# Performance work log

Measured on AMD Instinct MI355X. Metric: run time of the kernel, lower is better.

## Reference

```python
import jax, jax.numpy as jnp
import numpy as np

D_MODEL = 1024
N_HEADS = 16
HEAD_DIM = D_MODEL // N_HEADS


def setup_inputs() -> dict:
    key = jax.random.key(0)
    ks = jax.random.split(key, 5)
    x = jax.random.normal(ks[0], (2, 2048, D_MODEL), dtype=jnp.float32)
    s = 1.0 / np.sqrt(D_MODEL)
    W_qkv = jax.random.normal(ks[1], (D_MODEL, 3 * D_MODEL), dtype=jnp.float32) * s
    b_qkv = jnp.zeros((3 * D_MODEL,), dtype=jnp.float32)
    W_proj = jax.random.normal(ks[2], (D_MODEL, D_MODEL), dtype=jnp.float32) * s
    b_proj = jnp.zeros((D_MODEL,), dtype=jnp.float32)
    return {"x": x, "W_qkv": W_qkv, "b_qkv": b_qkv, "W_proj": W_proj, "b_proj": b_proj}


def reference(x, W_qkv, b_qkv, W_proj, b_proj):
    b, t, c = x.shape
    qkv = x @ W_qkv + b_qkv  # [b,t,3c]
    q, k, v = jnp.split(qkv, 3, axis=-1)
    # [b, h, t, d]
    q = q.reshape(b, t, N_HEADS, HEAD_DIM).transpose(0, 2, 1, 3)
    k = k.reshape(b, t, N_HEADS, HEAD_DIM).transpose(0, 2, 1, 3)
    v = v.reshape(b, t, N_HEADS, HEAD_DIM).transpose(0, 2, 1, 3)
    att = jnp.einsum('bhqd,bhkd->bhqk', q, k) / np.sqrt(HEAD_DIM)
    causal = jnp.tril(jnp.ones((t, t), dtype=bool))  # [t,t]
    att = jnp.where(causal[None, None], att, -jnp.inf)
    att = jax.nn.softmax(att, axis=-1)
    out = jnp.einsum('bhqk,bhkd->bhqd', att, v)  # [b,h,t,d]
    out = out.transpose(0, 2, 1, 3).reshape(b, t, c)
    return out @ W_proj + b_proj
```

## Files before the change

kernel.cpp:

```cpp
#include <hip/hip_runtime.h>
#include <hip/hip_bf16.h>

#define NB 2
#define NH 16
#define HD 64
#define DM 1024
#define TT 2048

typedef __attribute__((ext_vector_type(4))) float f32x4;
typedef __attribute__((ext_vector_type(8))) short bf16x8;

__device__ __forceinline__ unsigned short f2bf(float f) {
  union { float f; unsigned int i; } x; x.f = f;
  unsigned int r = x.i + 0x7fffu + ((x.i >> 16) & 1u);
  return (unsigned short)(r >> 16);
}

__device__ __forceinline__ unsigned int cvtpk(float lo, float hi) {
  unsigned int r;
  asm("v_cvt_pk_bf16_f32 %0, %1, %2" : "=v"(r) : "v"(lo), "v"(hi));
  return r;
}

__device__ __forceinline__ void async16(unsigned short* lds_base, const unsigned short* g) {
  __builtin_amdgcn_global_load_lds(
      (const __attribute__((address_space(1))) void*)g,
      (__attribute__((address_space(3))) void*)lds_base, 16, 0, 0);
}

__global__ __launch_bounds__(256)
void prep_kernel(const float* __restrict__ x, unsigned short* __restrict__ xbf,
                 const float* __restrict__ Wqkv, unsigned short* __restrict__ WqkvT,
                 const float* __restrict__ Wproj, unsigned short* __restrict__ WprojT)
{
  __shared__ unsigned short T[64][72];
  const int bid = blockIdx.x;
  const int t = threadIdx.x;

  if (bid < 2048) {
    const int i = bid * 256 + t;
    const f32x4 a = *(const f32x4*)(x + (size_t)i * 8);
    const f32x4 b = *(const f32x4*)(x + (size_t)i * 8 + 4);
    uint4 o;
    o.x = f2bf(a.x) | ((unsigned)f2bf(a.y) << 16);
    o.y = f2bf(a.z) | ((unsigned)f2bf(a.w) << 16);
    o.z = f2bf(b.x) | ((unsigned)f2bf(b.y) << 16);
    o.w = f2bf(b.z) | ((unsigned)f2bf(b.w) << 16);
    *(uint4*)(xbf + (size_t)i * 8) = o;
    return;
  }

  const float* W;
  unsigned short* WT;
  int n0, k0, N;
  if (bid < 2048 + 768) {
    const int li = bid - 2048;
    W = Wqkv; WT = WqkvT; N = 3 * DM;
    n0 = (li % 48) * 64; k0 = (li / 48) * 64;
  } else {
    const int li = bid - 2816;
    W = Wproj; WT = WprojT; N = DM;
    n0 = (li % 16) * 64; k0 = (li / 16) * 64;
  }
  const int r = t >> 2;
  const int c = (t & 3) * 16;
  const float* src = W + (size_t)(k0 + r) * N + n0 + c;
  #pragma unroll
  for (int s = 0; s < 4; ++s) {
    const f32x4 v = *(const f32x4*)(src + s * 4);
    T[c + s*4 + 0][r] = f2bf(v.x);
    T[c + s*4 + 1][r] = f2bf(v.y);
    T[c + s*4 + 2][r] = f2bf(v.z);
    T[c + s*4 + 3][r] = f2bf(v.w);
  }
  __syncthreads();
  unsigned short* dst = WT + (size_t)(n0 + r) * DM + k0 + c;
  *(uint4*)(dst)     = *(const uint4*)(&T[r][c]);
  *(uint4*)(dst + 8) = *(const uint4*)(&T[r][c + 8]);
}

template<int MODE>
__global__ __launch_bounds__(256)
void gemm_bf16(const unsigned short* __restrict__ A, const unsigned short* __restrict__ BT,
               const float* __restrict__ bias, void* __restrict__ Cout,
               int M, int N, int K)
{
  __shared__ unsigned short As[128 * 32];
  __shared__ unsigned short Bs[128 * 32];
  const int tid = threadIdx.x;
  const int lane = tid & 63;
  const int w = tid >> 6;
  const int wr = w >> 1, wc = w & 1;
  const int l15 = lane & 15, g = lane >> 4;

  const int gx = gridDim.x;
  const int li = blockIdx.y * gx + blockIdx.x;
  const int chunk = (gx * gridDim.y) >> 3;
  const int tile = (li & 7) * chunk + (li >> 3);
  const int m0 = (tile / gx) * 128;
  const int n0 = (tile % gx) * 128;

  f32x4 acc[4][4] = {};

  const int ar0 = tid >> 2,          as0 = (tid & 3) * 8;
  const int ar1 = (256 + tid) >> 2;
  const unsigned short* A0 = A + (size_t)(m0 + ar0) * K + as0;
  const unsigned short* A1 = A + (size_t)(m0 + ar1) * K + as0;
  const unsigned short* B0 = BT + (size_t)(n0 + ar0) * K + as0;
  const unsigned short* B1 = BT + (size_t)(n0 + ar1) * K + as0;
  unsigned short* AsW0 = &As[(0 * 256 + w * 64) * 8];
  unsigned short* AsW1 = &As[(1 * 256 + w * 64) * 8];
  unsigned short* BsW0 = &Bs[(0 * 256 + w * 64) * 8];
  unsigned short* BsW1 = &Bs[(1 * 256 + w * 64) * 8];

  for (int k0 = 0; k0 < K; k0 += 32) {
    async16(AsW0, A0 + k0);
    async16(AsW1, A1 + k0);
    async16(BsW0, B0 + k0);
    async16(BsW1, B1 + k0);
    __syncthreads();

    bf16x8 af[4], bfv[4];
    #pragma unroll
    for (int i = 0; i < 4; ++i)
      af[i] = *(const bf16x8*)(&As[(wr * 64 + i * 16 + l15) * 32 + g * 8]);
    #pragma unroll
    for (int j = 0; j < 4; ++j)
      bfv[j] = *(const bf16x8*)(&Bs[(wc * 64 + j * 16 + l15) * 32 + g * 8]);
    #pragma unroll
    for (int i = 0; i < 4; ++i)
      #pragma unroll
      for (int j = 0; j < 4; ++j)
        acc[i][j] = __builtin_amdgcn_mfma_f32_16x16x32_bf16(af[i], bfv[j], acc[i][j], 0, 0, 0);
    __syncthreads();
  }

  #pragma unroll
  for (int i = 0; i < 4; ++i) {
    #pragma unroll
    for (int j = 0; j < 4; ++j) {
      #pragma unroll
      for (int e = 0; e < 4; ++e) {
        const int row = m0 + wr * 64 + i * 16 + g * 4 + e;
        const int col = n0 + wc * 64 + j * 16 + l15;
        float val = acc[i][j][e] + bias[col];
        if (MODE == 0) {
          const int which = col >> 10;
          if (which == 0) val *= 0.125f;
          const int rem = col & 1023;
          const int hh = rem >> 6, dd = rem & 63;
          const int bb = row >> 11, tt = row & 2047;
          ((unsigned short*)Cout)[((((size_t)which * NB + bb) * NH + hh) * TT + tt) * HD + dd] = f2bf(val);
        } else {
          ((float*)Cout)[(size_t)row * N + col] = val;
        }
      }
    }
  }
}

__global__ __launch_bounds__(512)
void attn_kernel(const unsigned short* __restrict__ qkv, unsigned short* __restrict__ attn_out)
{
  __shared__ unsigned short Ksm[64 * 72];
  __shared__ unsigned short VTsm[64 * 70];
  __shared__ unsigned short Psm[8][32 * 72];

  const int tid = threadIdx.x;
  const int lane = tid & 63;
  const int wv = tid >> 6;
  const int l15 = lane & 15;
  const int g = lane >> 4;

  const int li = blockIdx.x;
  const int xcd = li & 7;
  const int j = li >> 3;
  const int bh = ((j >> 3) << 3) | xcd;
  const int ip = j & 7;

  const int qlo0 = ip * 128;
  const int qhi0 = (15 - ip) * 128;

  const size_t base = (size_t)bh * TT * HD;
  const unsigned short* Qg = qkv + base;
  const unsigned short* Kg = qkv + (size_t)NB * NH * TT * HD + base;
  const unsigned short* Vg = qkv + (size_t)2 * NB * NH * TT * HD + base;

  const int qw_lo = qlo0 + wv * 16;
  const int qw_hi = qhi0 + wv * 16;
  const bf16x8 qlf0 = *(const bf16x8*)(Qg + (size_t)(qw_lo + l15) * HD + g * 8);
  const bf16x8 qlf1 = *(const bf16x8*)(Qg + (size_t)(qw_lo + l15) * HD + 32 + g * 8);
  const bf16x8 qhf0 = *(const bf16x8*)(Qg + (size_t)(qw_hi + l15) * HD + g * 8);
  const bf16x8 qhf1 = *(const bf16x8*)(Qg + (size_t)(qw_hi + l15) * HD + 32 + g * 8);

  f32x4 olo[4] = {}, ohi[4] = {};
  float llo = 0.f, lhi = 0.f;

  const bool kRole = (wv < 4);
  const int krow = (tid & 255) >> 2;
  const int kseg = (tid & 3) * 16;
  const int vt   = tid & 255;
  const int vr0  = (vt >> 4) * 4;
  const int vc0  = (vt & 15) * 4;

  const int nt    = 32 - 2 * ip;
  const int lo_nt = 2 * ip + 2;

  uint4 st0, st1;
  {
    if (kRole) {
      const unsigned short* kp = Kg + (size_t)krow * HD + kseg;
      st0 = *(const uint4*)(kp);
      st1 = *(const uint4*)(kp + 8);
    } else {
      const uint2 a = *(const uint2*)(Vg + (size_t)(vr0 + 0) * HD + vc0);
      const uint2 b = *(const uint2*)(Vg + (size_t)(vr0 + 1) * HD + vc0);
      const uint2 c = *(const uint2*)(Vg + (size_t)(vr0 + 2) * HD + vc0);
      const uint2 d = *(const uint2*)(Vg + (size_t)(vr0 + 3) * HD + vc0);
      st0.x = a.x; st0.y = a.y; st0.z = b.x; st0.w = b.y;
      st1.x = c.x; st1.y = c.y; st1.z = d.x; st1.w = d.y;
    }
  }

  for (int t = 0; t < nt; ++t) {
    const int t0 = t * 64;
    const bool lo_act = (t < lo_nt);
    __syncthreads();
    if (kRole) {
      *(uint4*)(&Ksm[krow * 72 + kseg])     = st0;
      *(uint4*)(&Ksm[krow * 72 + kseg + 8]) = st1;
    } else {
      unsigned short r0[4] = {(unsigned short)(st0.x & 0xffffu), (unsigned short)(st0.x >> 16),
                              (unsigned short)(st0.y & 0xffffu), (unsigned short)(st0.y >> 16)};
      unsigned short r1[4] = {(unsigned short)(st0.z & 0xffffu), (unsigned short)(st0.z >> 16),
                              (unsigned short)(st0.w & 0xffffu), (unsigned short)(st0.w >> 16)};
      unsigned short r2[4] = {(unsigned short)(st1.x & 0xffffu), (unsigned short)(st1.x >> 16),
                              (unsigned short)(st1.y & 0xffffu), (unsigned short)(st1.y >> 16)};
      unsigned short r3[4] = {(unsigned short)(st1.z & 0xffffu), (unsigned short)(st1.z >> 16),
                              (unsigned short)(st1.w & 0xffffu), (unsigned short)(st1.w >> 16)};
      #pragma unroll
      for (int c2 = 0; c2 < 4; ++c2) {
        ushort4 col;
        col.x = r0[c2]; col.y = r1[c2]; col.z = r2[c2]; col.w = r3[c2];
        *(ushort4*)(&VTsm[(vc0 + c2) * 70 + vr0]) = col;
      }
    }
    __syncthreads();

    if (t + 1 < nt) {
      const int t1 = t0 + 64;
      if (kRole) {
        const unsigned short* kp = Kg + (size_t)(t1 + krow) * HD + kseg;
        st0 = *(const uint4*)(kp);
        st1 = *(const uint4*)(kp + 8);
      } else {
        const uint2 a = *(const uint2*)(Vg + (size_t)(t1 + vr0 + 0) * HD + vc0);
        const uint2 b = *(const uint2*)(Vg + (size_t)(t1 + vr0 + 1) * HD + vc0);
        const uint2 c = *(const uint2*)(Vg + (size_t)(t1 + vr0 + 2) * HD + vc0);
        const uint2 d = *(const uint2*)(Vg + (size_t)(t1 + vr0 + 3) * HD + vc0);
        st0.x = a.x; st0.y = a.y; st0.z = b.x; st0.w = b.y;
        st1.x = c.x; st1.y = c.y; st1.z = d.x; st1.w = d.y;
      }
    }

    f32x4 shiT[4] = {}, sloT[4] = {};
    __builtin_amdgcn_s_setprio(1);
    #pragma unroll
    for (int b = 0; b < 4; ++b) {
      const bf16x8 kf0 = *(const bf16x8*)(&Ksm[(b * 16 + l15) * 72 + g * 8]);
      const bf16x8 kf1 = *(const bf16x8*)(&Ksm[(b * 16 + l15) * 72 + 32 + g * 8]);
      shiT[b] = __builtin_amdgcn_mfma_f32_16x16x32_bf16(kf0, qhf0, shiT[b], 0, 0, 0);
      shiT[b] = __builtin_amdgcn_mfma_f32_16x16x32_bf16(kf1, qhf1, shiT[b], 0, 0, 0);
      if (lo_act) {
        sloT[b] = __builtin_amdgcn_mfma_f32_16x16x32_bf16(kf0, qlf0, sloT[b], 0, 0, 0);
        sloT[b] = __builtin_amdgcn_mfma_f32_16x16x32_bf16(kf1, qlf1, sloT[b], 0, 0, 0);
      }
    }
    __builtin_amdgcn_s_setprio(0);

    if (t0 + 63 > qw_hi) {
      #pragma unroll
      for (int b = 0; b < 4; ++b)
        #pragma unroll
        for (int e = 0; e < 4; ++e)
          if (t0 + b * 16 + 4 * g + e > qw_hi + l15) shiT[b][e] = -INFINITY;
    }
    if (lo_act && t0 + 63 > qw_lo) {
      #pragma unroll
      for (int b = 0; b < 4; ++b)
        #pragma unroll
        for (int e = 0; e < 4; ++e)
          if (t0 + b * 16 + 4 * g + e > qw_lo + l15) sloT[b][e] = -INFINITY;
    }

    #pragma unroll
    for (int b = 0; b < 4; ++b) {
      const float p0 = __expf(shiT[b][0]);
      const float p1 = __expf(shiT[b][1]);
      const float p2 = __expf(shiT[b][2]);
      const float p3 = __expf(shiT[b][3]);
      lhi += (p0 + p1) + (p2 + p3);
      uint2 wd; wd.x = cvtpk(p0, p1); wd.y = cvtpk(p2, p3);
      *(uint2*)(&Psm[wv][(16 + l15) * 72 + b * 16 + 4 * g]) = wd;
    }
    if (lo_act) {
      #pragma unroll
      for (int b = 0; b < 4; ++b) {
        const float p0 = __expf(sloT[b][0]);
        const float p1 = __expf(sloT[b][1]);
        const float p2 = __expf(sloT[b][2]);
        const float p3 = __expf(sloT[b][3]);
        llo += (p0 + p1) + (p2 + p3);
        uint2 wd; wd.x = cvtpk(p0, p1); wd.y = cvtpk(p2, p3);
        *(uint2*)(&Psm[wv][l15 * 72 + b * 16 + 4 * g]) = wd;
      }
    }

    __builtin_amdgcn_s_setprio(1);
    #pragma unroll
    for (int c = 0; c < 2; ++c) {
      const bf16x8 pfh = *(const bf16x8*)(&Psm[wv][(16 + l15) * 72 + c * 32 + g * 8]);
      bf16x8 pfl;
      if (lo_act) pfl = *(const bf16x8*)(&Psm[wv][l15 * 72 + c * 32 + g * 8]);
      #pragma unroll
      for (int db = 0; db < 4; ++db) {
        const bf16x8 vf = *(const bf16x8*)(&VTsm[(db * 16 + l15) * 70 + c * 32 + g * 8]);
        ohi[db] = __builtin_amdgcn_mfma_f32_16x16x32_bf16(pfh, vf, ohi[db], 0, 0, 0);
        if (lo_act) olo[db] = __builtin_amdgcn_mfma_f32_16x16x32_bf16(pfl, vf, olo[db], 0, 0, 0);
      }
    }
    __builtin_amdgcn_s_setprio(0);
  }

  lhi += __shfl_xor(lhi, 16, 64);
  lhi += __shfl_xor(lhi, 32, 64);
  llo += __shfl_xor(llo, 16, 64);
  llo += __shfl_xor(llo, 32, 64);

  const int bb = bh >> 4;
  const int hh = bh & 15;
  #pragma unroll
  for (int e = 0; e < 4; ++e) {
    const float invh = 1.f / __shfl(lhi, 4 * g + e, 64);
    const float invl = 1.f / __shfl(llo, 4 * g + e, 64);
    const int qh = qw_hi + 4 * g + e;
    const int ql = qw_lo + 4 * g + e;
    #pragma unroll
    for (int db = 0; db < 4; ++db) {
      attn_out[(size_t)(bb * TT + qh) * DM + hh * HD + db * 16 + l15] = f2bf(ohi[db][e] * invh);
      attn_out[(size_t)(bb * TT + ql) * DM + hh * HD + db * 16 + l15] = f2bf(olo[db][e] * invl);
    }
  }
}

extern "C" void kernel_launch(void* const* d_in, const int* in_sizes, int n_in,
                              void* d_out, int out_size, void* d_ws, size_t ws_size,
                              hipStream_t stream)
{
  const float* x     = (const float*)d_in[0];
  const float* Wqkv  = (const float*)d_in[1];
  const float* bqkv  = (const float*)d_in[2];
  const float* Wproj = (const float*)d_in[3];
  const float* bproj = (const float*)d_in[4];

  const size_t qkv_elems = (size_t)3 * NB * NH * TT * HD;
  unsigned short* qkv_ws  = (unsigned short*)d_ws;
  unsigned short* WqkvT   = qkv_ws + qkv_elems;
  unsigned short* WprojT  = WqkvT + (size_t)3 * DM * DM;
  unsigned short* xbf     = WprojT + (size_t)DM * DM;
  unsigned short* attn_ws = xbf;

  hipLaunchKernelGGL(prep_kernel, dim3(3072, 1, 1), dim3(256), 0, stream,
                     x, xbf, Wqkv, WqkvT, Wproj, WprojT);
  hipLaunchKernelGGL((gemm_bf16<0>), dim3(3 * DM / 128, NB * TT / 128, 1), dim3(256), 0, stream,
                     xbf, WqkvT, bqkv, (void*)qkv_ws, NB * TT, 3 * DM, DM);
  hipLaunchKernelGGL(attn_kernel, dim3(256, 1, 1), dim3(512), 0, stream,
                     qkv_ws, attn_ws);
  hipLaunchKernelGGL((gemm_bf16<1>), dim3(DM / 128, NB * TT / 128, 1), dim3(256), 0, stream,
                     attn_ws, WprojT, bproj, d_out, NB * TT, DM, DM);
}
```

Baseline: 133.9 us.

## Split paired causal query tiles into separate blocks and skip fully masked key tiles

The attention kernel used to give each block a low and a high 128-row query tile so causal work was balanced. Now each block handles one query tile, the grid doubles to 512 blocks, and the heavy tiles are scheduled first. Each wave also skips the QK/PV work for key tiles that lie entirely above its own 16 rows. This adds parallelism and removes masked compute, but the K/V tiles are loaded into LDS twice as often overall, and block costs become uneven.

```diff
diff --git a/kernel.cpp b/kernel.cpp
--- a/kernel.cpp
+++ b/kernel.cpp
@@ -164,7 +164,7 @@
 {
   __shared__ unsigned short Ksm[64 * 72];
   __shared__ unsigned short VTsm[64 * 70];
-  __shared__ unsigned short Psm[8][32 * 72];
+  __shared__ unsigned short Psm[8][16 * 72];
 
   const int tid = threadIdx.x;
   const int lane = tid & 63;
@@ -174,27 +174,25 @@
 
   const int li = blockIdx.x;
   const int xcd = li & 7;
-  const int j = li >> 3;
+  const int r = li >> 3;
+  const int halfid = r >> 5;
+  const int j = r & 31;
   const int bh = ((j >> 3) << 3) | xcd;
-  const int ip = j & 7;
-
-  const int qlo0 = ip * 128;
-  const int qhi0 = (15 - ip) * 128;
+  const int jj = j & 7;
+  const int qt = halfid ? (7 - jj) : (8 + jj);
+  const int q0 = qt * 128;
 
   const size_t base = (size_t)bh * TT * HD;
   const unsigned short* Qg = qkv + base;
   const unsigned short* Kg = qkv + (size_t)NB * NH * TT * HD + base;
   const unsigned short* Vg = qkv + (size_t)2 * NB * NH * TT * HD + base;
 
-  const int qw_lo = qlo0 + wv * 16;
-  const int qw_hi = qhi0 + wv * 16;
-  const bf16x8 qlf0 = *(const bf16x8*)(Qg + (size_t)(qw_lo + l15) * HD + g * 8);
-  const bf16x8 qlf1 = *(const bf16x8*)(Qg + (size_t)(qw_lo + l15) * HD + 32 + g * 8);
-  const bf16x8 qhf0 = *(const bf16x8*)(Qg + (size_t)(qw_hi + l15) * HD + g * 8);
-  const bf16x8 qhf1 = *(const bf16x8*)(Qg + (size_t)(qw_hi + l15) * HD + 32 + g * 8);
-
-  f32x4 olo[4] = {}, ohi[4] = {};
-  float llo = 0.f, lhi = 0.f;
+  const int qw = q0 + wv * 16;
+  const bf16x8 qf0 = *(const bf16x8*)(Qg + (size_t)(qw + l15) * HD + g * 8);
+  const bf16x8 qf1 = *(const bf16x8*)(Qg + (size_t)(qw + l15) * HD + 32 + g * 8);
+
+  f32x4 o[4] = {};
+  float lsum = 0.f;
 
   const bool kRole = (wv < 4);
   const int krow = (tid & 255) >> 2;
@@ -203,8 +201,7 @@
   const int vr0  = (vt >> 4) * 4;
   const int vc0  = (vt & 15) * 4;
 
-  const int nt    = 32 - 2 * ip;
-  const int lo_nt = 2 * ip + 2;
+  const int nt = 2 * qt + 2;
 
   uint4 st0, st1;
   {
@@ -224,7 +221,6 @@
 
   for (int t = 0; t < nt; ++t) {
     const int t0 = t * 64;
-    const bool lo_act = (t < lo_nt);
     __syncthreads();
     if (kRole) {
       *(uint4*)(&Ksm[krow * 72 + kseg])     = st0;
@@ -263,93 +259,63 @@
       }
     }
 
-    f32x4 shiT[4] = {}, sloT[4] = {};
-    __builtin_amdgcn_s_setprio(1);
-    #pragma unroll
-    for (int b = 0; b < 4; ++b) {
-      const bf16x8 kf0 = *(const bf16x8*)(&Ksm[(b * 16 + l15) * 72 + g * 8]);
-      const bf16x8 kf1 = *(const bf16x8*)(&Ksm[(b * 16 + l15) * 72 + 32 + g * 8]);
-      shiT[b] = __builtin_amdgcn_mfma_f32_16x16x32_bf16(kf0, qhf0, shiT[b], 0, 0, 0);
-      shiT[b] = __builtin_amdgcn_mfma_f32_16x16x32_bf16(kf1, qhf1, shiT[b], 0, 0, 0);
-      if (lo_act) {
-        sloT[b] = __builtin_amdgcn_mfma_f32_16x16x32_bf16(kf0, qlf0, sloT[b], 0, 0, 0);
-        sloT[b] = __builtin_amdgcn_mfma_f32_16x16x32_bf16(kf1, qlf1, sloT[b], 0, 0, 0);
-      }
-    }
-    __builtin_amdgcn_s_setprio(0);
-
-    if (t0 + 63 > qw_hi) {
-      #pragma unroll
-      for (int b = 0; b < 4; ++b)
+    if (t0 <= qw + 15) {
+      f32x4 sT[4] = {};
+      __builtin_amdgcn_s_setprio(1);
+      #pragma unroll
+      for (int b = 0; b < 4; ++b) {
+        const bf16x8 kf0 = *(const bf16x8*)(&Ksm[(b * 16 + l15) * 72 + g * 8]);
+        const bf16x8 kf1 = *(const bf16x8*)(&Ksm[(b * 16 + l15) * 72 + 32 + g * 8]);
+        sT[b] = __builtin_amdgcn_mfma_f32_16x16x32_bf16(kf0, qf0, sT[b], 0, 0, 0);
+        sT[b] = __builtin_amdgcn_mfma_f32_16x16x32_bf16(kf1, qf1, sT[b], 0, 0, 0);
+      }
+      __builtin_amdgcn_s_setprio(0);
+
+      if (t0 + 63 > qw) {
         #pragma unroll
-        for (int e = 0; e < 4; ++e)
-          if (t0 + b * 16 + 4 * g + e > qw_hi + l15) shiT[b][e] = -INFINITY;
-    }
-    if (lo_act && t0 + 63 > qw_lo) {
-      #pragma unroll
-      for (int b = 0; b < 4; ++b)
-        #pragma unroll
-        for (int e = 0; e < 4; ++e)
-          if (t0 + b * 16 + 4 * g + e > qw_lo + l15) sloT[b][e] = -INFINITY;
-    }
-
-    #pragma unroll
-    for (int b = 0; b < 4; ++b) {
-      const float p0 = __expf(shiT[b][0]);
-      const float p1 = __expf(shiT[b][1]);
-      const float p2 = __expf(shiT[b][2]);
-      const float p3 = __expf(shiT[b][3]);
-      lhi += (p0 + p1) + (p2 + p3);
-      uint2 wd; wd.x = cvtpk(p0, p1); wd.y = cvtpk(p2, p3);
-      *(uint2*)(&Psm[wv][(16 + l15) * 72 + b * 16 + 4 * g]) = wd;
-    }
-    if (lo_act) {
+        for (int b = 0; b < 4; ++b)
+          #pragma unroll
+          for (int e = 0; e < 4; ++e)
+            if (t0 + b * 16 + 4 * g + e > qw + l15) sT[b][e] = -INFINITY;
+      }
+
       #pragma unroll
       for (int b = 0; b < 4; ++b) {
-        const float p0 = __expf(sloT[b][0]);
-        const float p1 = __expf(sloT[b][1]);
-        const float p2 = __expf(sloT[b][2]);
-        const float p3 = __expf(sloT[b][3]);
-        llo += (p0 + p1) + (p2 + p3);
+        const float p0 = __expf(sT[b][0]);
+        const float p1 = __expf(sT[b][1]);
+        const float p2 = __expf(sT[b][2]);
+        const float p3 = __expf(sT[b][3]);
+        lsum += (p0 + p1) + (p2 + p3);
         uint2 wd; wd.x = cvtpk(p0, p1); wd.y = cvtpk(p2, p3);
         *(uint2*)(&Psm[wv][l15 * 72 + b * 16 + 4 * g]) = wd;
       }
-    }
-
-    __builtin_amdgcn_s_setprio(1);
-    #pragma unroll
-    for (int c = 0; c < 2; ++c) {
-      const bf16x8 pfh = *(const bf16x8*)(&Psm[wv][(16 + l15) * 72 + c * 32 + g * 8]);
-      bf16x8 pfl;
-      if (lo_act) pfl = *(const bf16x8*)(&Psm[wv][l15 * 72 + c * 32 + g * 8]);
-      #pragma unroll
-      for (int db = 0; db < 4; ++db) {
-        const bf16x8 vf = *(const bf16x8*)(&VTsm[(db * 16 + l15) * 70 + c * 32 + g * 8]);
-        ohi[db] = __builtin_amdgcn_mfma_f32_16x16x32_bf16(pfh, vf, ohi[db], 0, 0, 0);
-        if (lo_act) olo[db] = __builtin_amdgcn_mfma_f32_16x16x32_bf16(pfl, vf, olo[db], 0, 0, 0);
-      }
-    }
-    __builtin_amdgcn_s_setprio(0);
-  }
-
-  lhi += __shfl_xor(lhi, 16, 64);
-  lhi += __shfl_xor(lhi, 32, 64);
-  llo += __shfl_xor(llo, 16, 64);
-  llo += __shfl_xor(llo, 32, 64);
+
+      __builtin_amdgcn_s_setprio(1);
+      #pragma unroll
+      for (int c = 0; c < 2; ++c) {
+        const bf16x8 pf = *(const bf16x8*)(&Psm[wv][l15 * 72 + c * 32 + g * 8]);
+        #pragma unroll
+        for (int db = 0; db < 4; ++db) {
+          const bf16x8 vf = *(const bf16x8*)(&VTsm[(db * 16 + l15) * 70 + c * 32 + g * 8]);
+          o[db] = __builtin_amdgcn_mfma_f32_16x16x32_bf16(pf, vf, o[db], 0, 0, 0);
+        }
+      }
+      __builtin_amdgcn_s_setprio(0);
+    }
+  }
+
+  lsum += __shfl_xor(lsum, 16, 64);
+  lsum += __shfl_xor(lsum, 32, 64);
 
   const int bb = bh >> 4;
   const int hh = bh & 15;
   #pragma unroll
   for (int e = 0; e < 4; ++e) {
-    const float invh = 1.f / __shfl(lhi, 4 * g + e, 64);
-    const float invl = 1.f / __shfl(llo, 4 * g + e, 64);
-    const int qh = qw_hi + 4 * g + e;
-    const int ql = qw_lo + 4 * g + e;
-    #pragma unroll
-    for (int db = 0; db < 4; ++db) {
-      attn_out[(size_t)(bb * TT + qh) * DM + hh * HD + db * 16 + l15] = f2bf(ohi[db][e] * invh);
-      attn_out[(size_t)(bb * TT + ql) * DM + hh * HD + db * 16 + l15] = f2bf(olo[db][e] * invl);
-    }
+    const float inv = 1.f / __shfl(lsum, 4 * g + e, 64);
+    const int q = qw + 4 * g + e;
+    #pragma unroll
+    for (int db = 0; db < 4; ++db)
+      attn_out[(size_t)(bb * TT + q) * DM + hh * HD + db * 16 + l15] = f2bf(o[db][e] * inv);
   }
 }
 
@@ -374,7 +340,7 @@
                      x, xbf, Wqkv, WqkvT, Wproj, WprojT);
   hipLaunchKernelGGL((gemm_bf16<0>), dim3(3 * DM / 128, NB * TT / 128, 1), dim3(256), 0, stream,
                      xbf, WqkvT, bqkv, (void*)qkv_ws, NB * TT, 3 * DM, DM);
-  hipLaunchKernelGGL(attn_kernel, dim3(256, 1, 1), dim3(512), 0, stream,
+  hipLaunchKernelGGL(attn_kernel, dim3(512, 1, 1), dim3(512), 0, stream,
                      qkv_ws, attn_ws);
   hipLaunchKernelGGL((gemm_bf16<1>), dim3(DM / 128, NB * TT / 128, 1), dim3(256), 0, stream,
                      attn_ws, WprojT, bproj, d_out, NB * TT, DM, DM);
```

After: 124.4 us. -7.1%, faster.
